# Optimization experiments

Measured on AMD Instinct MI355X. Metric: run time of the kernel, lower is better.

The kernel has to match this reference:

```python
import jax, jax.numpy as jnp
import numpy as np

N_NODES = 50000   # gates in the circuit batch
N_HOPS = 100000   # number of k-hop cones
MAX_PI = 8        # max PIs per hop (padded, masked via stats == -1)
D = 128           # token_emb / hidden
D_FF = 4 * D      # cls_head hidden width (512)
TT = 64           # max_tt_len -> logits width
LN_EPS = 1e-5


def setup_inputs() -> dict:
    key = jax.random.key(0)
    ks = jax.random.split(key, 8)
    hf = jax.random.normal(ks[0], (N_NODES, D), jnp.float32)
    all_hop_pi = jax.random.randint(ks[1], (N_HOPS, MAX_PI), 0, N_NODES)
    # stats in {-1, 0, 1}; -1 marks an invalid (padded) PI slot
    all_hop_pi_stats = jax.random.randint(ks[2], (N_HOPS, MAX_PI), 0, 3) - 1
    all_hop_po = jax.random.randint(ks[3], (N_HOPS,), 0, N_NODES)
    w_q = jax.random.normal(ks[4], (D,), jnp.float32) / np.sqrt(D)
    W1 = jax.random.normal(ks[5], (D, D_FF), jnp.float32) / np.sqrt(D)
    b1 = jnp.zeros((D_FF,), jnp.float32)
    gamma = jnp.ones((D_FF,), jnp.float32)
    beta = jnp.zeros((D_FF,), jnp.float32)
    W2 = jax.random.normal(ks[6], (D_FF, TT), jnp.float32) / np.sqrt(D_FF)
    b2 = jnp.zeros((TT,), jnp.float32)
    return {
        'hf': hf, 'w_q': w_q, 'W1': W1, 'b1': b1, 'gamma': gamma,
        'beta': beta, 'W2': W2, 'b2': b2,
        'all_hop_pi': all_hop_pi, 'all_hop_pi_stats': all_hop_pi_stats,
        'all_hop_po': all_hop_po,
    }


def reference(hf, w_q, W1, b1, gamma, beta, W2, b2,
              all_hop_pi, all_hop_pi_stats, all_hop_po):
    # Per-hop gather: valid PI embeddings + PO embedding -> [H, P+1, D]
    pi_tok = hf[all_hop_pi]                       # [H, P, D]
    po_tok = hf[all_hop_po][:, None, :]           # [H, 1, D]
    tokens = jnp.concatenate([pi_tok, po_tok], axis=1)
    valid = jnp.concatenate(
        [all_hop_pi_stats != -1,
         jnp.ones((all_hop_po.shape[0], 1), bool)], axis=1)  # [H, P+1]
    # tf_Pooling: masked single-query attention pooling over the ragged set
    scores = jnp.einsum('hpd,d->hp', tokens, w_q) / jnp.sqrt(jnp.float32(D))
    scores = jnp.where(valid, scores, jnp.float32(-1e30))
    attn = jax.nn.softmax(scores, axis=-1)
    hop_hf = jnp.einsum('hp,hpd->hd', attn, tokens)  # [H, D]
    # cls_head: Linear(D, 4D) -> ReLU -> LayerNorm(4D) -> Linear(4D, TT)
    h = jax.nn.relu(hop_hf @ W1 + b1)
    mu = jnp.mean(h, axis=-1, keepdims=True)
    var = jnp.var(h, axis=-1, keepdims=True)
    h = (h - mu) * jax.lax.rsqrt(var + LN_EPS) * gamma + beta
    logits = h @ W2 + b2                           # [H, TT]
    return logits
```

## Files before the change

kernel.cpp:

```cpp
#include <hip/hip_runtime.h>
#include <hip/hip_bf16.h>
#include <math.h>

#define DIM 128
#define DFF 512
#define TTW 64
#define NPI 8
#define NTOK 9
#define TILE_H 32

typedef __attribute__((ext_vector_type(8))) short short8;
typedef __attribute__((ext_vector_type(4))) float float4v;

__device__ __forceinline__ float bf16lo_f32(unsigned u) {
    union { unsigned u; float f; } v; v.u = u << 16;
    return v.f;
}
__device__ __forceinline__ float bf16hi_f32(unsigned u) {
    union { unsigned u; float f; } v; v.u = u & 0xffff0000u;
    return v.f;
}
__device__ __forceinline__ unsigned pk_bf16(float a, float b) {
    __hip_bfloat162 h = __float22bfloat162_rn(float2{a, b});
    union { __hip_bfloat162 h; unsigned u; } cv; cv.h = h;
    return cv.u;
}

__global__ __launch_bounds__(256)
void prep_k(const float* __restrict__ hf, const float* __restrict__ W1,
            const float* __restrict__ W2, const float* __restrict__ gamma,
            const float* __restrict__ beta, const float* __restrict__ b2,
            unsigned short* __restrict__ hf2, unsigned short* __restrict__ w1t,
            unsigned short* __restrict__ w2g,
            float* __restrict__ C1, float* __restrict__ C2,
            int n_hf, int B_HF)
{
    __shared__ float tile[32][33];
    const int b = blockIdx.x, t = threadIdx.x;
    if (b < B_HF) {
        int i = (b * 256 + t) * 8;
        if (i < n_hf) {
            float4v v0 = *(const float4v*)(hf + i);
            float4v v1 = *(const float4v*)(hf + i + 4);
            uint4 o;
            o.x = pk_bf16(v0[0], v0[1]);
            o.y = pk_bf16(v0[2], v0[3]);
            o.z = pk_bf16(v1[0], v1[1]);
            o.w = pk_bf16(v1[2], v1[3]);
            *(uint4*)(hf2 + i) = o;
        }
    } else if (b < B_HF + 64) {
        const int tb = b - B_HF;
        const int r0 = (tb & 3) * 32, c0 = (tb >> 2) * 32;
        const int ty = t >> 3, tx = t & 7;
        *(float4v*)&tile[ty][tx * 4] = *(const float4v*)(W1 + (r0 + ty) * DFF + c0 + tx * 4);
        __syncthreads();
        uint2 o;
        o.x = pk_bf16(tile[tx * 4 + 0][ty], tile[tx * 4 + 1][ty]);
        o.y = pk_bf16(tile[tx * 4 + 2][ty], tile[tx * 4 + 3][ty]);
        *(uint2*)(w1t + (c0 + ty) * DIM + r0 + tx * 4) = o;
    } else if (b < B_HF + 96) {
        const int tb = b - B_HF - 64;
        const int r0 = (tb & 15) * 32, c0 = (tb >> 4) * 32;
        const int ty = t >> 3, tx = t & 7;
        const float g = gamma[r0 + ty];
        float4v v = *(const float4v*)(W2 + (r0 + ty) * TTW + c0 + tx * 4);
        v[0] *= g; v[1] *= g; v[2] *= g; v[3] *= g;
        *(float4v*)&tile[ty][tx * 4] = v;
        __syncthreads();
        uint2 o;
        o.x = pk_bf16(tile[tx * 4 + 0][ty], tile[tx * 4 + 1][ty]);
        o.y = pk_bf16(tile[tx * 4 + 2][ty], tile[tx * 4 + 3][ty]);
        *(uint2*)(w2g + (c0 + ty) * DFF + r0 + tx * 4) = o;
    } else {
        if (t < TTW) {
            float c1 = 0.f, c2 = 0.f;
            for (int k = 0; k < DFF; ++k) {
                float w = W2[k * TTW + t];
                c1 += gamma[k] * w;
                c2 += beta[k] * w;
            }
            C1[t] = c1;
            C2[t] = b2[t] + c2;
        }
    }
}

__global__ __launch_bounds__(256)
void pool_k(const unsigned short* __restrict__ hf2,
            const float* __restrict__ w_q,
            const int* __restrict__ pi,
            const int* __restrict__ stats,
            const int* __restrict__ po,
            uint2* apool,
            int H)
{
    const int t = threadIdx.x;
    const int g = t >> 5, l = t & 31;
    const int hop = blockIdx.x * 8 + g;
    if (hop >= H) return;

    const float4v wq4 = *(const float4v*)(w_q + l * 4);
    const int4 p0 = *(const int4*)(pi + hop * NPI);
    const int4 p1 = *(const int4*)(pi + hop * NPI + 4);
    const int4 s0 = *(const int4*)(stats + hop * NPI);
    const int4 s1 = *(const int4*)(stats + hop * NPI + 4);
    const int ipo = po[hop];

    uint2 tu[NTOK];
    tu[0] = *(const uint2*)(hf2 + (size_t)p0.x * DIM + l * 4);
    tu[1] = *(const uint2*)(hf2 + (size_t)p0.y * DIM + l * 4);
    tu[2] = *(const uint2*)(hf2 + (size_t)p0.z * DIM + l * 4);
    tu[3] = *(const uint2*)(hf2 + (size_t)p0.w * DIM + l * 4);
    tu[4] = *(const uint2*)(hf2 + (size_t)p1.x * DIM + l * 4);
    tu[5] = *(const uint2*)(hf2 + (size_t)p1.y * DIM + l * 4);
    tu[6] = *(const uint2*)(hf2 + (size_t)p1.z * DIM + l * 4);
    tu[7] = *(const uint2*)(hf2 + (size_t)p1.w * DIM + l * 4);
    tu[8] = *(const uint2*)(hf2 + (size_t)ipo * DIM + l * 4);

    const unsigned vm = (s0.x != -1 ? 1u   : 0u) | (s0.y != -1 ? 2u   : 0u)
                      | (s0.z != -1 ? 4u   : 0u) | (s0.w != -1 ? 8u   : 0u)
                      | (s1.x != -1 ? 16u  : 0u) | (s1.y != -1 ? 32u  : 0u)
                      | (s1.z != -1 ? 64u  : 0u) | (s1.w != -1 ? 128u : 0u)
                      | 256u;

    float sc[NTOK];
    #pragma unroll
    for (int p = 0; p < NTOK; ++p) {
        float x0 = bf16lo_f32(tu[p].x), x1 = bf16hi_f32(tu[p].x);
        float x2 = bf16lo_f32(tu[p].y), x3 = bf16hi_f32(tu[p].y);
        sc[p] = x0 * wq4[0] + x1 * wq4[1] + x2 * wq4[2] + x3 * wq4[3];
    }
    #pragma unroll
    for (int m = 1; m < 32; m <<= 1) {
        #pragma unroll
        for (int p = 0; p < NTOK; ++p) sc[p] += __shfl_xor(sc[p], m);
    }
    const float isd = 0.08838834764831845f;
    float mx = -1e30f;
    #pragma unroll
    for (int p = 0; p < NTOK; ++p) {
        sc[p] = ((vm >> p) & 1u) ? sc[p] * isd : -1e30f;
        mx = fmaxf(mx, sc[p]);
    }
    float se = 0.f;
    #pragma unroll
    for (int p = 0; p < NTOK; ++p) { sc[p] = __expf(sc[p] - mx); se += sc[p]; }
    const float inv = 1.f / se;
    float a0 = 0.f, a1 = 0.f, a2 = 0.f, a3 = 0.f;
    #pragma unroll
    for (int p = 0; p < NTOK; ++p) {
        const float a = sc[p] * inv;
        a0 += a * bf16lo_f32(tu[p].x);  a1 += a * bf16hi_f32(tu[p].x);
        a2 += a * bf16lo_f32(tu[p].y);  a3 += a * bf16hi_f32(tu[p].y);
    }
    uint2 o;
    o.x = pk_bf16(a0, a1);
    o.y = pk_bf16(a2, a3);
    apool[(size_t)hop * 32 + l] = o;
}

__global__ __launch_bounds__(256)
void mlp_k(const uint4* apool4,
           const unsigned short* __restrict__ w1t,
           const float* __restrict__ b1,
           const unsigned short* __restrict__ w2g,
           const float* __restrict__ C1,
           const float* __restrict__ C2,
           float* out,
           int H)
{
    __shared__ __align__(16) unsigned short Apool[TILE_H][DIM + 8];
    __shared__ __align__(16) unsigned short Hsm[TILE_H][256 + 8];
    __shared__ float part[2][16][4][2];
    __shared__ float2 mursm[TILE_H];

    const int t    = threadIdx.x;
    const int lane = t & 63;
    const int w    = t >> 6;
    const int row  = lane & 15;
    const int quad = lane >> 4;
    const int hop0 = blockIdx.x * TILE_H;

    #pragma unroll
    for (int j = t; j < 512; j += 256) {
        int gr = hop0 + (j >> 4);
        if (gr >= H) gr = H - 1;
        uint4 v = apool4[(size_t)gr * 16 + (j & 15)];
        *(uint4*)&Apool[j >> 4][(j & 15) * 8] = v;
    }
    __syncthreads();

    float4v acc[8][2];
    #pragma unroll
    for (int mt = 0; mt < 8; ++mt) {
        acc[mt][0] = (float4v){0.f, 0.f, 0.f, 0.f};
        acc[mt][1] = (float4v){0.f, 0.f, 0.f, 0.f};
    }
    {
        short8 bfr[2][4];
        #pragma unroll
        for (int ks = 0; ks < 4; ++ks) {
            const int k0 = ks * 32 + quad * 8;
            #pragma unroll
            for (int ht = 0; ht < 2; ++ht)
                bfr[ht][ks] = *(const short8*)&Apool[ht * 16 + row][k0];
        }
        #pragma unroll
        for (int mt = 0; mt < 8; ++mt) {
            const unsigned short* wrow = w1t + (size_t)(mt * 64 + w * 16 + row) * DIM;
            #pragma unroll
            for (int ks = 0; ks < 4; ++ks) {
                short8 afr = *(const short8*)(wrow + ks * 32 + quad * 8);
                acc[mt][0] = __builtin_amdgcn_mfma_f32_16x16x32_bf16(afr, bfr[0][ks], acc[mt][0], 0, 0, 0);
                acc[mt][1] = __builtin_amdgcn_mfma_f32_16x16x32_bf16(afr, bfr[1][ks], acc[mt][1], 0, 0, 0);
            }
        }
    }
    float sum0 = 0.f, ssq0 = 0.f, sum1 = 0.f, ssq1 = 0.f;
    uint2 pk[8][2];
    #pragma unroll
    for (int mt = 0; mt < 8; ++mt) {
        const int nb = mt * 64 + w * 16 + quad * 4;
        const float4v bias = *(const float4v*)(b1 + nb);
        float o0[4], o1[4];
        #pragma unroll
        for (int r = 0; r < 4; ++r) {
            o0[r] = fmaxf(acc[mt][0][r] + bias[r], 0.f);
            o1[r] = fmaxf(acc[mt][1][r] + bias[r], 0.f);
            sum0 += o0[r];  ssq0 += o0[r] * o0[r];
            sum1 += o1[r];  ssq1 += o1[r] * o1[r];
        }
        pk[mt][0].x = pk_bf16(o0[0], o0[1]);  pk[mt][0].y = pk_bf16(o0[2], o0[3]);
        pk[mt][1].x = pk_bf16(o1[0], o1[1]);  pk[mt][1].y = pk_bf16(o1[2], o1[3]);
    }
    #pragma unroll
    for (int m = 16; m <= 32; m <<= 1) {
        sum0 += __shfl_xor(sum0, m);  ssq0 += __shfl_xor(ssq0, m);
        sum1 += __shfl_xor(sum1, m);  ssq1 += __shfl_xor(ssq1, m);
    }
    if (lane < 16) {
        part[0][row][w][0] = sum0;  part[0][row][w][1] = ssq0;
        part[1][row][w][0] = sum1;  part[1][row][w][1] = ssq1;
    }
    __syncthreads();
    {
        const float invn = 1.f / (float)DFF;
        float mu0, rs0, mu1, rs1;
        {
            float S = 0.f, Q = 0.f;
            #pragma unroll
            for (int ww = 0; ww < 4; ++ww) { S += part[0][row][ww][0]; Q += part[0][row][ww][1]; }
            mu0 = S * invn;  rs0 = rsqrtf(Q * invn - mu0 * mu0 + 1e-5f);
        }
        {
            float S = 0.f, Q = 0.f;
            #pragma unroll
            for (int ww = 0; ww < 4; ++ww) { S += part[1][row][ww][0]; Q += part[1][row][ww][1]; }
            mu1 = S * invn;  rs1 = rsqrtf(Q * invn - mu1 * mu1 + 1e-5f);
        }
        if (t < 16) {
            mursm[t]      = float2{mu0, rs0};
            mursm[16 + t] = float2{mu1, rs1};
        }
    }
    {
        float4v acc2[2];
        acc2[0] = (float4v){0.f,0.f,0.f,0.f};
        acc2[1] = (float4v){0.f,0.f,0.f,0.f};
        #pragma unroll
        for (int c = 0; c < 2; ++c) {
            #pragma unroll
            for (int m4 = 0; m4 < 4; ++m4) {
                const int col = m4 * 64 + w * 16 + quad * 4;
                *(uint2*)&Hsm[0 * 16 + row][col] = pk[c * 4 + m4][0];
                *(uint2*)&Hsm[1 * 16 + row][col] = pk[c * 4 + m4][1];
            }
            __syncthreads();
            const unsigned short* w2row = w2g + (size_t)(w * 16 + row) * DFF + c * 256;
            #pragma unroll
            for (int ks = 0; ks < 8; ++ks) {
                const int k0 = ks * 32 + quad * 8;
                short8 bfr = *(const short8*)(w2row + k0);
                #pragma unroll
                for (int mt = 0; mt < 2; ++mt) {
                    short8 afr = *(const short8*)&Hsm[mt * 16 + row][k0];
                    acc2[mt] = __builtin_amdgcn_mfma_f32_16x16x32_bf16(
                        afr, bfr, acc2[mt], 0, 0, 0);
                }
            }
            if (c == 0) __syncthreads();
        }
        const int tt = w * 16 + row;
        const float c1v = C1[tt];
        const float c2v = C2[tt];
        #pragma unroll
        for (int mt = 0; mt < 2; ++mt) {
            #pragma unroll
            for (int r = 0; r < 4; ++r) {
                const int hl = mt * 16 + quad * 4 + r;
                int hop = hop0 + hl;
                if (hop < H) {
                    float2 mr = mursm[hl];
                    out[(size_t)hop * TTW + tt] = mr.y * (acc2[mt][r] - mr.x * c1v) + c2v;
                }
            }
        }
    }
}

extern "C" void kernel_launch(void* const* d_in, const int* in_sizes, int n_in,
                              void* d_out, int out_size, void* d_ws, size_t ws_size,
                              hipStream_t stream) {
    const float* hf    = (const float*)d_in[0];
    const float* w_q   = (const float*)d_in[1];
    const float* W1    = (const float*)d_in[2];
    const float* b1    = (const float*)d_in[3];
    const float* gamma = (const float*)d_in[4];
    const float* beta  = (const float*)d_in[5];
    const float* W2    = (const float*)d_in[6];
    const float* b2    = (const float*)d_in[7];
    const int* pi      = (const int*)d_in[8];
    const int* stats   = (const int*)d_in[9];
    const int* po      = (const int*)d_in[10];
    float* out         = (float*)d_out;

    const int n_hf = in_sizes[0];
    const int H    = in_sizes[10];
    const int ntiles = (H + TILE_H - 1) / TILE_H;

    char* ws = (char*)d_ws;
    unsigned short* w1t = (unsigned short*)ws;
    unsigned short* w2g = (unsigned short*)(ws + 131072);
    unsigned short* hf2 = (unsigned short*)(ws + 196608);
    float* C1 = (float*)(ws + 196608 + (size_t)n_hf * 2);
    float* C2 = C1 + TTW;

    const int B_HF = (n_hf + 2047) / 2048;
    hipLaunchKernelGGL(prep_k, dim3(B_HF + 97), dim3(256), 0, stream,
                       hf, W1, W2, gamma, beta, b2, hf2, w1t, w2g, C1, C2, n_hf, B_HF);
    hipLaunchKernelGGL(pool_k, dim3((H + 7) / 8), dim3(256), 0, stream,
                       hf2, w_q, pi, stats, po, (uint2*)d_out, H);
    hipLaunchKernelGGL(mlp_k, dim3(ntiles), dim3(256), 0, stream,
                       (const uint4*)d_out, w1t, b1, w2g, C1, C2, out, H);
}
```

Measured before the change: 235.0 us.

## Shrink MLP hop tile to 16 rows to cut registers and raise occupancy

The fused MLP kernel now handles 16 hops per block instead of 32. This holds 4 float4 accumulators at a time instead of 16, writes the whole 512-wide hidden row to shared memory once, and uses a single 16-step second GEMM with one fewer barrier. Launch-bounds minimum-occupancy hints are added to both the pooling and MLP kernels. The aim is lower register pressure and more resident waves. The cost is that each block still streams the full W1 and W2 weights, so weight traffic from L2 roughly doubles because there are twice as many blocks.

```diff
diff --git a/kernel.cpp b/kernel.cpp
--- a/kernel.cpp
+++ b/kernel.cpp
@@ -7,7 +7,7 @@
 #define TTW 64
 #define NPI 8
 #define NTOK 9
-#define TILE_H 32
+#define TILE_M 16
 
 typedef __attribute__((ext_vector_type(8))) short short8;
 typedef __attribute__((ext_vector_type(4))) float float4v;
@@ -86,7 +86,7 @@
     }
 }
 
-__global__ __launch_bounds__(256)
+__global__ __launch_bounds__(256, 4)
 void pool_k(const unsigned short* __restrict__ hf2,
             const float* __restrict__ w_q,
             const int* __restrict__ pi,
@@ -160,7 +160,7 @@
     apool[(size_t)hop * 32 + l] = o;
 }
 
-__global__ __launch_bounds__(256)
+__global__ __launch_bounds__(256, 3)
 void mlp_k(const uint4* apool4,
            const unsigned short* __restrict__ w1t,
            const float* __restrict__ b1,
@@ -170,140 +170,105 @@
            float* out,
            int H)
 {
-    __shared__ __align__(16) unsigned short Apool[TILE_H][DIM + 8];
-    __shared__ __align__(16) unsigned short Hsm[TILE_H][256 + 8];
-    __shared__ float part[2][16][4][2];
-    __shared__ float2 mursm[TILE_H];
+    __shared__ __align__(16) unsigned short Apool[TILE_M][DIM + 8];
+    __shared__ __align__(16) unsigned short Hsm[TILE_M][DFF + 8];
+    __shared__ float part[16][4][2];
+    __shared__ float2 mursm[TILE_M];
 
     const int t    = threadIdx.x;
     const int lane = t & 63;
     const int w    = t >> 6;
     const int row  = lane & 15;
     const int quad = lane >> 4;
-    const int hop0 = blockIdx.x * TILE_H;
-
-    #pragma unroll
-    for (int j = t; j < 512; j += 256) {
-        int gr = hop0 + (j >> 4);
+    const int hop0 = blockIdx.x * TILE_M;
+
+    {
+        int gr = hop0 + (t >> 4);
         if (gr >= H) gr = H - 1;
-        uint4 v = apool4[(size_t)gr * 16 + (j & 15)];
-        *(uint4*)&Apool[j >> 4][(j & 15) * 8] = v;
+        uint4 v = apool4[(size_t)gr * 16 + (t & 15)];
+        *(uint4*)&Apool[t >> 4][(t & 15) * 8] = v;
     }
     __syncthreads();
 
-    float4v acc[8][2];
-    #pragma unroll
-    for (int mt = 0; mt < 8; ++mt) {
-        acc[mt][0] = (float4v){0.f, 0.f, 0.f, 0.f};
-        acc[mt][1] = (float4v){0.f, 0.f, 0.f, 0.f};
-    }
-    {
-        short8 bfr[2][4];
-        #pragma unroll
-        for (int ks = 0; ks < 4; ++ks) {
-            const int k0 = ks * 32 + quad * 8;
-            #pragma unroll
-            for (int ht = 0; ht < 2; ++ht)
-                bfr[ht][ks] = *(const short8*)&Apool[ht * 16 + row][k0];
-        }
-        #pragma unroll
-        for (int mt = 0; mt < 8; ++mt) {
+    short8 bfr[4];
+    #pragma unroll
+    for (int ks = 0; ks < 4; ++ks)
+        bfr[ks] = *(const short8*)&Apool[row][ks * 32 + quad * 8];
+
+    float sum = 0.f, ssq = 0.f;
+    uint2 pk[8];
+    #pragma unroll
+    for (int gmt = 0; gmt < 2; ++gmt) {
+        float4v acc4[4];
+        #pragma unroll
+        for (int m4 = 0; m4 < 4; ++m4)
+            acc4[m4] = (float4v){0.f, 0.f, 0.f, 0.f};
+        #pragma unroll
+        for (int m4 = 0; m4 < 4; ++m4) {
+            const int mt = gmt * 4 + m4;
             const unsigned short* wrow = w1t + (size_t)(mt * 64 + w * 16 + row) * DIM;
             #pragma unroll
             for (int ks = 0; ks < 4; ++ks) {
                 short8 afr = *(const short8*)(wrow + ks * 32 + quad * 8);
-                acc[mt][0] = __builtin_amdgcn_mfma_f32_16x16x32_bf16(afr, bfr[0][ks], acc[mt][0], 0, 0, 0);
-                acc[mt][1] = __builtin_amdgcn_mfma_f32_16x16x32_bf16(afr, bfr[1][ks], acc[mt][1], 0, 0, 0);
+                acc4[m4] = __builtin_amdgcn_mfma_f32_16x16x32_bf16(afr, bfr[ks], acc4[m4], 0, 0, 0);
             }
         }
-    }
-    float sum0 = 0.f, ssq0 = 0.f, sum1 = 0.f, ssq1 = 0.f;
-    uint2 pk[8][2];
-    #pragma unroll
-    for (int mt = 0; mt < 8; ++mt) {
-        const int nb = mt * 64 + w * 16 + quad * 4;
-        const float4v bias = *(const float4v*)(b1 + nb);
-        float o0[4], o1[4];
-        #pragma unroll
-        for (int r = 0; r < 4; ++r) {
-            o0[r] = fmaxf(acc[mt][0][r] + bias[r], 0.f);
-            o1[r] = fmaxf(acc[mt][1][r] + bias[r], 0.f);
-            sum0 += o0[r];  ssq0 += o0[r] * o0[r];
-            sum1 += o1[r];  ssq1 += o1[r] * o1[r];
-        }
-        pk[mt][0].x = pk_bf16(o0[0], o0[1]);  pk[mt][0].y = pk_bf16(o0[2], o0[3]);
-        pk[mt][1].x = pk_bf16(o1[0], o1[1]);  pk[mt][1].y = pk_bf16(o1[2], o1[3]);
+        #pragma unroll
+        for (int m4 = 0; m4 < 4; ++m4) {
+            const int mt = gmt * 4 + m4;
+            const int nb = mt * 64 + w * 16 + quad * 4;
+            const float4v bias = *(const float4v*)(b1 + nb);
+            float o0[4];
+            #pragma unroll
+            for (int r = 0; r < 4; ++r) {
+                o0[r] = fmaxf(acc4[m4][r] + bias[r], 0.f);
+                sum += o0[r];  ssq += o0[r] * o0[r];
+            }
+            pk[mt].x = pk_bf16(o0[0], o0[1]);
+            pk[mt].y = pk_bf16(o0[2], o0[3]);
+        }
     }
     #pragma unroll
     for (int m = 16; m <= 32; m <<= 1) {
-        sum0 += __shfl_xor(sum0, m);  ssq0 += __shfl_xor(ssq0, m);
-        sum1 += __shfl_xor(sum1, m);  ssq1 += __shfl_xor(ssq1, m);
+        sum += __shfl_xor(sum, m);  ssq += __shfl_xor(ssq, m);
     }
     if (lane < 16) {
-        part[0][row][w][0] = sum0;  part[0][row][w][1] = ssq0;
-        part[1][row][w][0] = sum1;  part[1][row][w][1] = ssq1;
-    }
+        part[row][w][0] = sum;  part[row][w][1] = ssq;
+    }
+    #pragma unroll
+    for (int mt = 0; mt < 8; ++mt)
+        *(uint2*)&Hsm[row][mt * 64 + w * 16 + quad * 4] = pk[mt];
     __syncthreads();
+    if (t < 16) {
+        float S = 0.f, Q = 0.f;
+        #pragma unroll
+        for (int ww = 0; ww < 4; ++ww) { S += part[t][ww][0]; Q += part[t][ww][1]; }
+        const float invn = 1.f / (float)DFF;
+        float mu = S * invn;
+        float rs = rsqrtf(Q * invn - mu * mu + 1e-5f);
+        mursm[t] = float2{mu, rs};
+    }
     {
-        const float invn = 1.f / (float)DFF;
-        float mu0, rs0, mu1, rs1;
-        {
-            float S = 0.f, Q = 0.f;
-            #pragma unroll
-            for (int ww = 0; ww < 4; ++ww) { S += part[0][row][ww][0]; Q += part[0][row][ww][1]; }
-            mu0 = S * invn;  rs0 = rsqrtf(Q * invn - mu0 * mu0 + 1e-5f);
-        }
-        {
-            float S = 0.f, Q = 0.f;
-            #pragma unroll
-            for (int ww = 0; ww < 4; ++ww) { S += part[1][row][ww][0]; Q += part[1][row][ww][1]; }
-            mu1 = S * invn;  rs1 = rsqrtf(Q * invn - mu1 * mu1 + 1e-5f);
-        }
-        if (t < 16) {
-            mursm[t]      = float2{mu0, rs0};
-            mursm[16 + t] = float2{mu1, rs1};
-        }
-    }
-    {
-        float4v acc2[2];
-        acc2[0] = (float4v){0.f,0.f,0.f,0.f};
-        acc2[1] = (float4v){0.f,0.f,0.f,0.f};
-        #pragma unroll
-        for (int c = 0; c < 2; ++c) {
-            #pragma unroll
-            for (int m4 = 0; m4 < 4; ++m4) {
-                const int col = m4 * 64 + w * 16 + quad * 4;
-                *(uint2*)&Hsm[0 * 16 + row][col] = pk[c * 4 + m4][0];
-                *(uint2*)&Hsm[1 * 16 + row][col] = pk[c * 4 + m4][1];
-            }
-            __syncthreads();
-            const unsigned short* w2row = w2g + (size_t)(w * 16 + row) * DFF + c * 256;
-            #pragma unroll
-            for (int ks = 0; ks < 8; ++ks) {
-                const int k0 = ks * 32 + quad * 8;
-                short8 bfr = *(const short8*)(w2row + k0);
-                #pragma unroll
-                for (int mt = 0; mt < 2; ++mt) {
-                    short8 afr = *(const short8*)&Hsm[mt * 16 + row][k0];
-                    acc2[mt] = __builtin_amdgcn_mfma_f32_16x16x32_bf16(
-                        afr, bfr, acc2[mt], 0, 0, 0);
-                }
-            }
-            if (c == 0) __syncthreads();
-        }
+        float4v acc2 = (float4v){0.f, 0.f, 0.f, 0.f};
+        const unsigned short* w2row = w2g + (size_t)(w * 16 + row) * DFF;
+        #pragma unroll
+        for (int ks = 0; ks < 16; ++ks) {
+            const int k0 = ks * 32 + quad * 8;
+            short8 bfr2 = *(const short8*)(w2row + k0);
+            short8 afr2 = *(const short8*)&Hsm[row][k0];
+            acc2 = __builtin_amdgcn_mfma_f32_16x16x32_bf16(afr2, bfr2, acc2, 0, 0, 0);
+        }
+        __syncthreads();
         const int tt = w * 16 + row;
         const float c1v = C1[tt];
         const float c2v = C2[tt];
         #pragma unroll
-        for (int mt = 0; mt < 2; ++mt) {
-            #pragma unroll
-            for (int r = 0; r < 4; ++r) {
-                const int hl = mt * 16 + quad * 4 + r;
-                int hop = hop0 + hl;
-                if (hop < H) {
-                    float2 mr = mursm[hl];
-                    out[(size_t)hop * TTW + tt] = mr.y * (acc2[mt][r] - mr.x * c1v) + c2v;
-                }
+        for (int r = 0; r < 4; ++r) {
+            const int hl = quad * 4 + r;
+            int hop = hop0 + hl;
+            if (hop < H) {
+                float2 mr = mursm[hl];
+                out[(size_t)hop * TTW + tt] = mr.y * (acc2[r] - mr.x * c1v) + c2v;
             }
         }
     }
@@ -327,7 +292,7 @@
 
     const int n_hf = in_sizes[0];
     const int H    = in_sizes[10];
-    const int ntiles = (H + TILE_H - 1) / TILE_H;
+    const int ntiles = (H + TILE_M - 1) / TILE_M;
 
     char* ws = (char*)d_ws;
     unsigned short* w1t = (unsigned short*)ws;
```

New measurement: 282.8 us. 1.2x slower.
